# Kernel optimization log

Hardware: AMD Instinct MI355X
Metric: run time of the kernel (lower is better)

Reference implementation:

```python
import jax, jax.numpy as jnp
import numpy as np
jax.config.update("jax_enable_x64", True)

MS_H = 10
MS_W = 10
EPS = 1e-8


def _window_mean(x, kh, kw):
    # x: [B, H, W]; VALID avg-pool with kernel (kh, kw), stride 1, via integral image
    c = jnp.cumsum(jnp.cumsum(x, axis=1), axis=2)
    c = jnp.pad(c, ((0, 0), (1, 0), (1, 0)))
    H, W = x.shape[1], x.shape[2]
    oh, ow = H - kh + 1, W - kw + 1
    s = (c[:, kh:kh + oh, kw:kw + ow] - c[:, :oh, kw:kw + ow]
         - c[:, kh:kh + oh, :ow] + c[:, :oh, :ow])
    return s / (kh * kw)


def _translate_bilinear(imgs, dy, dx):
    # imgs: [B, H, W]; out[b,i,j] = imgs[b, i - dy[b], j - dx[b]] (bilinear, zero fill)
    B, H, W = imgs.shape
    yq = jnp.arange(H, dtype=imgs.dtype)[None, :, None] - dy[:, None, None]
    xq = jnp.arange(W, dtype=imgs.dtype)[None, None, :] - dx[:, None, None]
    y0 = jnp.floor(yq); x0 = jnp.floor(xq)
    wy = yq - y0;       wx = xq - x0
    y0i = y0.astype(jnp.int32); x0i = x0.astype(jnp.int32)
    b = jnp.arange(B)[:, None, None]
    def samp(yi, xi):
        valid = (yi >= 0) & (yi < H) & (xi >= 0) & (xi < W)
        v = imgs[b, jnp.clip(yi, 0, H - 1), jnp.clip(xi, 0, W - 1)]
        return jnp.where(valid, v, jnp.zeros((), imgs.dtype))
    v00 = samp(y0i, x0i);     v01 = samp(y0i, x0i + 1)
    v10 = samp(y0i + 1, x0i); v11 = samp(y0i + 1, x0i + 1)
    return (v00 * (1 - wy) * (1 - wx) + v01 * (1 - wy) * wx
            + v10 * wy * (1 - wx) + v11 * wy * wx)


def _motion_correct(fr, template):
    # fr: [1, B, H, W, 1] float32; template: [H, W] float32
    B = fr.shape[1]
    H, W = template.shape
    mx, my = H // 2, W // 2
    # --- template normalization ---
    t_zm = template - jnp.mean(template)
    t_var = jnp.sum(jnp.square(t_zm)) + EPS
    target_freq = jnp.fft.fft2(t_zm.astype(jnp.complex128))            # [H, W]
    imgs = fr[0, :, :, :, 0]                                           # [B, H, W]
    imgs_zm = imgs - jnp.mean(imgs, axis=(1, 2), keepdims=True)
    # --- local statistics (avg_pool2d VALID, kernel = template minus shift margins) ---
    kh, kw = H - 2 * MS_W, W - 2 * MS_H
    m1 = _window_mean(imgs, kh, kw)                                    # [B, 2mw+1, 2mh+1]
    m2 = _window_mean(jnp.square(imgs), kh, kw)
    imgs_var = m2 - jnp.square(m1) / (kh * kw) + EPS
    imgs_var = jnp.where(imgs_var < 0, 0.0, imgs_var)
    denominator = jnp.sqrt(t_var * imgs_var)
    # --- FFT cross-correlation (fft3d over batch+spatial, exactly as the TF code) ---
    fr_freq = jnp.fft.fftn(imgs_zm.astype(jnp.complex128), axes=(0, 1, 2))
    img_product = fr_freq * jnp.conj(target_freq)[None]
    cc = jnp.abs(jnp.fft.ifftn(img_product, axes=(0, 1, 2))).astype(jnp.float32)
    rolled = jnp.roll(cc, (B, mx, my), axis=(0, 1, 2))
    nom = rolled[:, mx - MS_W:mx + MS_W + 1, my - MS_H:my + MS_H + 1]
    ncc = nom / denominator
    ncc = jnp.where(jnp.isnan(ncc), 0.0, ncc)                          # [B, 2mw+1, 2mh+1]
    # --- integer peak ---
    flat = ncc.reshape(B, -1)
    am = jnp.argmax(flat, axis=1)
    shx = am // (2 * MS_H + 1)
    shy = am % (2 * MS_H + 1)
    sh_x_n = -(shx - MS_H).astype(jnp.float32)
    sh_y_n = -(shy - MS_W).astype(jnp.float32)
    # --- log-parabolic sub-pixel refinement ---
    l = jnp.log(ncc)
    b = jnp.arange(B)
    lxm1 = l[b, shx - 1, shy]; lxp1 = l[b, shx + 1, shy]
    lym1 = l[b, shx, shy - 1]; lyp1 = l[b, shx, shy + 1]
    lc4 = 4.0 * l[b, shx, shy]
    sh_x_n = sh_x_n - (lxm1 - lxp1) / (2 * lxm1 - lc4 + 2 * lxp1)
    sh_y_n = sh_y_n - (lym1 - lyp1) / (2 * lym1 - lc4 + 2 * lyp1)
    # --- bilinear translate; tfa translations = [sh_y (dx, width), sh_x (dy, height)] ---
    warped = _translate_bilinear(imgs, sh_x_n, sh_y_n)                 # [B, H, W]
    return jnp.transpose(warped, (0, 2, 1)).reshape(B, H * W)


def setup_inputs() -> dict:
    H = W = 512
    B = 32
    k1, k2, k3 = jax.random.split(jax.random.key(0), 3)
    # smooth (low-pass) random template so the NCC peak is smooth/positive around its max
    noise = jax.random.normal(k1, (H, W))
    f = jnp.sqrt(jnp.fft.fftfreq(H)[:, None] ** 2 + jnp.fft.fftfreq(W)[None, :] ** 2)
    lp = (f < 0.05).astype(jnp.complex128)
    template = jnp.real(jnp.fft.ifft2(jnp.fft.fft2(noise) * lp))
    template = (template / template.std()).astype(jnp.float32)
    # frames: template shifted by small random integer offsets + noise
    shifts = jax.random.randint(k2, (B, 2), -5, 6)
    frames = jax.vmap(lambda s: jnp.roll(template, (s[0], s[1]), axis=(0, 1)))(shifts)
    frames = frames + 0.05 * jax.random.normal(k3, (B, H, W), dtype=jnp.float32)
    fr = frames[None, :, :, :, None].astype(jnp.float32)
    return {"fr": fr, "template": template}


def reference(fr, template):
    return _motion_correct(fr, template)
```

## Files before the change

### kernel.cpp

```cpp
#include <hip/hip_runtime.h>
#include <math.h>

#define HH 512
#define WW 512
#define NPIX (HH*WW)
#define NB 32
#define NS 21
#define KWIN 492
#define NKB 512
#define MT28 28
#define PARTSZ (MT28*32*16)

typedef __attribute__((ext_vector_type(8))) short short8;
typedef __attribute__((ext_vector_type(8))) unsigned short ushort8;
typedef __attribute__((ext_vector_type(4))) float floatx4;

__device__ __forceinline__ unsigned short f2bf(float f) {
    unsigned u = __float_as_uint(f);
    unsigned r = (u + 0x7fffu + ((u >> 16) & 1u)) >> 16;
    return (unsigned short)r;
}

__global__ __launch_bounds__(256) void stage1(
    const float* __restrict__ fr, const float* __restrict__ tpl,
    unsigned short* __restrict__ tplv,
    float* __restrict__ I1, float* __restrict__ I2,
    double* __restrict__ sum1, double* __restrict__ sum2)
{
    int blk = blockIdx.x;
    int t   = threadIdx.x;
    if (blk < 512) {
        int id = blk;
        int b  = id >> 4;
        int yg = id & 15;
        int y0, ny;
        if (yg < 8) { y0 = 20 + 30 * yg; ny = 30; }
        else        { y0 = 260 + 29 * (yg - 8); ny = 29; }
        const float* img = fr + (size_t)b * NPIX;
        int xa = t, xb = t + 256;
        float s1a = 0.f, s2a = 0.f, s1b = 0.f, s2b = 0.f;
        for (int y = y0; y < y0 + ny; ++y) {
            float va = img[(size_t)y * WW + xa];
            float vb = img[(size_t)y * WW + xb];
            s1a += va; s2a += va * va;
            s1b += vb; s2b += vb * vb;
        }
        atomicAdd(&I1[b * WW + xa], s1a); atomicAdd(&I2[b * WW + xa], s2a);
        atomicAdd(&I1[b * WW + xb], s1b); atomicAdd(&I2[b * WW + xb], s2b);
    } else if (blk < 520) {
        int gq = blk - 512;
        int y0 = 64 * gq;
        int xa = t, xb = t + 256;
        float s1a = 0.f, s2a = 0.f, s1b = 0.f, s2b = 0.f;
        for (int y = y0; y < y0 + 64; ++y) {
            float va = tpl[(size_t)y * WW + xa];
            float vb = tpl[(size_t)y * WW + xb];
            s1a += va; s2a += va * va;
            s1b += vb; s2b += vb * vb;
        }
        double d1 = (double)s1a + (double)s1b;
        double d2 = (double)s2a + (double)s2b;
        for (int off = 32; off; off >>= 1) {
            d1 += __shfl_down(d1, off);
            d2 += __shfl_down(d2, off);
        }
        __shared__ double r1[4], r2[4];
        int lane = t & 63, wv = t >> 6;
        if (lane == 0) { r1[wv] = d1; r2[wv] = d2; }
        __syncthreads();
        if (t == 0) {
            atomicAdd(&sum1[32], r1[0] + r1[1] + r1[2] + r1[3]);
            atomicAdd(&sum2[32], r2[0] + r2[1] + r2[2] + r2[3]);
        }
    } else {
        int blk2 = blk - 520;
        int dv   = blk2 / 34;
        int prg  = blk2 % 34;
        int prEnd = min(16 * prg + 16, 532);
        int x2 = 2 * t;
        for (int pr = 16 * prg; pr < prEnd; ++pr) {
            int sy = (pr + 502) & 511;
            const float* srow = tpl + (size_t)sy * WW;
            unsigned short* drow = tplv + ((size_t)dv * 532 + pr) * 512;
            int sx0 = (x2     - dv + 522) & 511;
            int sx1 = (x2 + 1 - dv + 522) & 511;
            ushort2 o;
            o.x = f2bf(srow[sx0]);
            o.y = f2bf(srow[sx1]);
            *(ushort2*)(drow + x2) = o;
        }
    }
}

__global__ __launch_bounds__(896) void corr_mfma(
    const float* __restrict__ fr,
    const unsigned short* __restrict__ tplv,
    float* __restrict__ part)
{
    __shared__ unsigned short Bs[16384];

    const int t   = threadIdx.x;
    const int l   = t & 63;
    const int wid = t >> 6;
    const int idx = blockIdx.x;
    const int kb  = ((idx & 7) << 6) | (idx >> 3);
    const int k0  = kb << 9;
    const int kg  = l >> 4;
    const int ln  = l & 15;

    for (int i = t; i < 4096; i += 896) {
        int frame = i >> 7;
        int q     = i & 127;
        float4 v = *(const float4*)(fr + (size_t)frame * NPIX + k0 + 4 * q);
        int k8 = q >> 1, j4 = (q & 1) * 4;
        ushort4 o;
        o.x = f2bf(v.x); o.y = f2bf(v.y); o.z = f2bf(v.z); o.w = f2bf(v.w);
        *(ushort4*)&Bs[(k8 * 32 + frame) * 8 + j4] = o;
    }

    const unsigned short* pA0;
    const unsigned short* pA1;
    {
        int m_g = 32 * wid + ln;
        int du  = (m_g * 1561) >> 15;
        int dv  = m_g - 21 * du;
        if (m_g >= 441) { du = 0; dv = 0; }
        pA0 = tplv + ((size_t)(dv * 532 + 20 - du) * 512 + 8 * kg + k0);
        m_g = 32 * wid + 16 + ln;
        du  = (m_g * 1561) >> 15;
        dv  = m_g - 21 * du;
        if (m_g >= 441) { du = 0; dv = 0; }
        pA1 = tplv + ((size_t)(dv * 532 + 20 - du) * 512 + 8 * kg + k0);
    }

    const unsigned short* lB = Bs + kg * 256 + ln * 8;

    __syncthreads();

    floatx4 acc00 = {}, acc01 = {}, acc10 = {}, acc11 = {};

#pragma unroll
    for (int ks = 0; ks < 16; ++ks) {
        short8 A0 = *(const short8*)pA0;
        short8 A1 = *(const short8*)pA1;
        short8 B0 = *(const short8*)(lB + ks * 1024);
        short8 B1 = *(const short8*)(lB + ks * 1024 + 128);
        acc00 = __builtin_amdgcn_mfma_f32_16x16x32_bf16(A0, B0, acc00, 0, 0, 0);
        acc01 = __builtin_amdgcn_mfma_f32_16x16x32_bf16(A0, B1, acc01, 0, 0, 0);
        acc10 = __builtin_amdgcn_mfma_f32_16x16x32_bf16(A1, B0, acc10, 0, 0, 0);
        acc11 = __builtin_amdgcn_mfma_f32_16x16x32_bf16(A1, B1, acc11, 0, 0, 0);
        pA0 += 32; pA1 += 32;
    }

    {
        size_t base = ((size_t)kb * MT28 + 2 * wid) * 32;
        floatx4* p;
        p = (floatx4*)(part + (base + ln)      * 16 + 4 * kg); *p = acc00;
        p = (floatx4*)(part + (base + 16 + ln) * 16 + 4 * kg); *p = acc01;
        p = (floatx4*)(part + (base + 32 + ln) * 16 + 4 * kg); *p = acc10;
        p = (floatx4*)(part + (base + 48 + ln) * 16 + 4 * kg); *p = acc11;
    }
}

__global__ __launch_bounds__(512) void reduce_stage2(
    const float* __restrict__ part, float* __restrict__ cc,
    const float* __restrict__ fr, const float* __restrict__ I1,
    const float* __restrict__ I2, double* __restrict__ sum1,
    const double* __restrict__ sum2, float* __restrict__ denom)
{
    __shared__ double wr1[NS][8], wr2[NS][8], wrT[8];
    __shared__ float  e1[NS][40], e2[NS][40];
    __shared__ double totals1[NS], totals2[NS];

    int blk = blockIdx.x;
    if (blk < 224) {
        int oct = blk / 28;
        int j   = (blk % 28) * 512 + threadIdx.x;
        const float* p = part + (size_t)(oct * 64) * PARTSZ + j;
        float s = 0.f;
#pragma unroll 8
        for (int i = 0; i < 64; ++i)
            s += p[(size_t)i * PARTSZ];
        int mr    = j & 15;
        int n     = (j >> 4) & 31;
        int mtile = j >> 9;
        int m = mtile * 16 + mr;
        if (m < 441)
            atomicAdd(&cc[(size_t)n * 441 + m], s);
        return;
    }

    int b = blk - 224;
    int x = threadIdx.x;
    const float* img = fr + (size_t)b * NPIX;
    float top[20], bot[20];
#pragma unroll
    for (int y = 0; y < 20; ++y) top[y] = img[(size_t)y * WW + x];
#pragma unroll
    for (int y = 0; y < 20; ++y) bot[y] = img[(size_t)(492 + y) * WW + x];

    float t1 = 0.f, t2 = 0.f, b1 = 0.f, b2 = 0.f;
#pragma unroll
    for (int y = 0; y < 20; ++y) {
        t1 += top[y]; t2 += top[y] * top[y];
        b1 += bot[y]; b2 += bot[y] * bot[y];
    }
    float i1 = I1[b * WW + x], i2 = I2[b * WW + x];
    int lane = x & 63, wv = x >> 6;

    double tot = (double)i1 + (double)t1 + (double)b1;
    for (int off = 32; off; off >>= 1) tot += __shfl_down(tot, off);
    if (lane == 0) wrT[wv] = tot;

    float s1 = i1 + t1, s2 = i2 + t2;
#pragma unroll
    for (int u = 0; u < NS; ++u) {
        if (u) {
            float a = top[u-1], c = bot[u-1];
            s1 += c - a;
            s2 += c * c - a * a;
        }
        double d1 = (double)s1, d2 = (double)s2;
        for (int off = 32; off; off >>= 1) {
            d1 += __shfl_down(d1, off);
            d2 += __shfl_down(d2, off);
        }
        if (lane == 0) { wr1[u][wv] = d1; wr2[u][wv] = d2; }
        if (x < 20)        { e1[u][x]       = s1; e2[u][x]       = s2; }
        else if (x >= 492) { e1[u][x - 472] = s1; e2[u][x - 472] = s2; }
    }
    __syncthreads();
    if (x == 0) {
        double s = 0.0;
        for (int i = 0; i < 8; ++i) s += wrT[i];
        sum1[b] = s;
    }
    if (x < NS) {
        double a = 0.0, c = 0.0;
        for (int i = 0; i < 8; ++i) { a += wr1[x][i]; c += wr2[x][i]; }
        totals1[x] = a; totals2[x] = c;
    }
    __syncthreads();
    if (x < NS * NS) {
        int u = x / NS, v = x - NS * u;
        double S1 = totals1[u], S2 = totals2[u];
        for (int j = 0; j < v; ++j)  { S1 -= (double)e1[u][j];      S2 -= (double)e2[u][j]; }
        for (int j = v; j < 20; ++j) { S1 -= (double)e1[u][20 + j]; S2 -= (double)e2[u][20 + j]; }
        const double inv = 1.0 / ((double)KWIN * (double)KWIN);
        double m1 = S1 * inv, m2 = S2 * inv;
        double var = m2 - (m1 * m1) * inv + 1e-8;
        if (var < 0.0) var = 0.0;
        double tv = sum2[32] - sum1[32] * sum1[32] * (1.0 / (double)NPIX) + 1e-8;
        denom[(size_t)b * NS * NS + x] = (float)sqrt(tv * var);
    }
}

__global__ __launch_bounds__(64) void argmax_kernel(
    const float* __restrict__ cc, const float* __restrict__ denom,
    const double* __restrict__ sum1, float* __restrict__ shifts)
{
    int b = blockIdx.x;
    const float* C = cc    + (size_t)b * NS * NS;
    const float* D = denom + (size_t)b * NS * NS;
    float corr = (float)(sum1[b] * sum1[32] * (1.0 / (double)NPIX));
    int l = threadIdx.x;
    float best = -1e30f; int bidx = NS * NS;
    for (int i = l; i < NS * NS; i += 64) {
        float v = fabsf(C[i] - corr) / D[i];
        if (v != v) v = 0.f;
        if (v > best) { best = v; bidx = i; }
    }
    for (int off = 32; off; off >>= 1) {
        float ov = __shfl_down(best, off);
        int   oi = __shfl_down(bidx, off);
        if (ov > best || (ov == best && oi < bidx)) { best = ov; bidx = oi; }
    }
    if (l == 0) {
        int shx = bidx / NS, shy = bidx % NS;
        auto nccAt = [&](int i, int j) -> float {
            i = (i < 0) ? i + NS : i; i = (i > NS - 1) ? NS - 1 : i;
            j = (j < 0) ? j + NS : j; j = (j > NS - 1) ? NS - 1 : j;
            float v = fabsf(C[i * NS + j] - corr) / D[i * NS + j];
            if (v != v) v = 0.f;
            return v;
        };
        float lc  = logf(nccAt(shx, shy));
        float lxm = logf(nccAt(shx - 1, shy));
        float lxp = logf(nccAt(shx + 1, shy));
        float lym = logf(nccAt(shx, shy - 1));
        float lyp = logf(nccAt(shx, shy + 1));
        float shxn = -(float)(shx - 10) - (lxm - lxp) / (2.f * lxm - 4.f * lc + 2.f * lxp);
        float shyn = -(float)(shy - 10) - (lym - lyp) / (2.f * lym - 4.f * lc + 2.f * lyp);
        shifts[b]      = shxn;
        shifts[32 + b] = shyn;
    }
}

__device__ __forceinline__ float samp(const float* __restrict__ img, int y, int x) {
    bool valid = (y >= 0) & (y < HH) & (x >= 0) & (x < WW);
    int yc = min(max(y, 0), HH - 1), xc = min(max(x, 0), WW - 1);
    float v = img[(size_t)yc * WW + xc];
    return valid ? v : 0.f;
}

__global__ __launch_bounds__(256) void warp_kernel(
    const float* __restrict__ fr, const float* __restrict__ shifts,
    float* __restrict__ out)
{
    int b  = blockIdx.z;
    int h0 = blockIdx.y * 32;
    int w0 = blockIdx.x * 32;
    float dy = shifts[b], dx = shifts[32 + b];
    const float* img = fr + (size_t)b * NPIX;
    __shared__ float tile[32][33];
    int tx = threadIdx.x & 31;
    int tz = threadIdx.x >> 5;
#pragma unroll
    for (int s = 0; s < 4; ++s) {
        int h = h0 + tz + 8 * s;
        int w = w0 + tx;
        float yq = (float)h - dy;
        float xq = (float)w - dx;
        float y0f = floorf(yq), x0f = floorf(xq);
        float wy = yq - y0f, wx = xq - x0f;
        int y0 = (int)y0f, x0 = (int)x0f;
        float v00 = samp(img, y0,     x0);
        float v01 = samp(img, y0,     x0 + 1);
        float v10 = samp(img, y0 + 1, x0);
        float v11 = samp(img, y0 + 1, x0 + 1);
        float val = v00 * (1.f - wy) * (1.f - wx) + v01 * (1.f - wy) * wx
                  + v10 * wy * (1.f - wx)         + v11 * wy * wx;
        tile[tz + 8 * s][tx] = val;
    }
    __syncthreads();
#pragma unroll
    for (int s = 0; s < 4; ++s) {
        int hh = tx;
        int ww = tz + 8 * s;
        out[(size_t)b * NPIX + (size_t)(w0 + ww) * HH + (h0 + hh)] = tile[hh][ww];
    }
}

extern "C" void kernel_launch(void* const* d_in, const int* in_sizes, int n_in,
                              void* d_out, int out_size, void* d_ws, size_t ws_size,
                              hipStream_t stream) {
    const float* fr  = (const float*)d_in[0];
    const float* tpl = (const float*)d_in[1];
    float* out = (float*)d_out;
    char* ws = (char*)d_ws;

    double* sum1    = (double*)(ws + 0);
    double* sum2    = (double*)(ws + 512);
    float*  cc      = (float*) (ws + 4096);
    float*  I1      = (float*) (ws + 61440);
    float*  I2      = (float*) (ws + 126976);
    float*  shifts  = (float*) (ws + 196608);
    float*  denom   = (float*) (ws + 200704);
    unsigned short* tplv = (unsigned short*)(ws + 262144);
    float*  part    = (float*) (ws + 16777216);

    hipMemsetAsync(ws, 0, 192512, stream);

    stage1       <<<1234, 256, 0, stream>>>(fr, tpl, tplv, I1, I2, sum1, sum2);
    corr_mfma    <<<512, 896, 0, stream>>>(fr, tplv, part);
    reduce_stage2<<<256, 512, 0, stream>>>(part, cc, fr, I1, I2, sum1, sum2, denom);
    argmax_kernel<<<32, 64, 0, stream>>>(cc, denom, sum1, shifts);
    warp_kernel  <<<dim3(16, 16, 32), 256, 0, stream>>>(fr, shifts, out);
}
```

Baseline: 167.1 us.

## Shrink shifted-template buffer, drop memset and atomics, fuse argmax into reduce

The 21 column-shifted bf16 template copies are replaced by two parity copies with a 544-wide padded row. The MFMA A-operand loads now use 4-byte loads so that unaligned offsets are handled. Column and template sums become per-block partials summed later, which removes the memset and the float atomics. The argmax kernel is merged into the reduce kernel through a global flag spin-wait on the 224 reduce blocks, which saves one launch. The spin-wait depends on co-residency of the reduce blocks and the per-batch argmax blocks, and the cross-block handoff adds a risk of deadlock or stalls.

```diff
diff --git a/kernel.cpp b/kernel.cpp
--- a/kernel.cpp
+++ b/kernel.cpp
@@ -7,12 +7,11 @@
 #define NB 32
 #define NS 21
 #define KWIN 492
-#define NKB 512
 #define MT28 28
 #define PARTSZ (MT28*32*16)
+#define TPLB_COPY 278528
 
 typedef __attribute__((ext_vector_type(8))) short short8;
-typedef __attribute__((ext_vector_type(8))) unsigned short ushort8;
 typedef __attribute__((ext_vector_type(4))) float floatx4;
 
 __device__ __forceinline__ unsigned short f2bf(float f) {
@@ -21,80 +20,79 @@
     return (unsigned short)r;
 }
 
-__global__ __launch_bounds__(256) void stage1(
+__device__ __forceinline__ short8 loadA(const unsigned short* p) {
+    union { short8 v; unsigned u[4]; } r;
+    const unsigned* q = (const unsigned*)p;
+    r.u[0] = q[0]; r.u[1] = q[1]; r.u[2] = q[2]; r.u[3] = q[3];
+    return r.v;
+}
+
+__global__ __launch_bounds__(512) void prep(
     const float* __restrict__ fr, const float* __restrict__ tpl,
-    unsigned short* __restrict__ tplv,
-    float* __restrict__ I1, float* __restrict__ I2,
-    double* __restrict__ sum1, double* __restrict__ sum2)
+    unsigned short* __restrict__ tplb,
+    float* __restrict__ I1p, float* __restrict__ I2p,
+    double* __restrict__ tplS1p, double* __restrict__ tplS2p,
+    int* __restrict__ flag)
 {
     int blk = blockIdx.x;
     int t   = threadIdx.x;
-    if (blk < 512) {
-        int id = blk;
-        int b  = id >> 4;
-        int yg = id & 15;
-        int y0, ny;
-        if (yg < 8) { y0 = 20 + 30 * yg; ny = 30; }
-        else        { y0 = 260 + 29 * (yg - 8); ny = 29; }
+    if (blk == 0 && t == 0) *flag = 0;
+
+    if (blk < 256) {
+        int b = blk >> 3, oct = blk & 7;
         const float* img = fr + (size_t)b * NPIX;
-        int xa = t, xb = t + 256;
-        float s1a = 0.f, s2a = 0.f, s1b = 0.f, s2b = 0.f;
-        for (int y = y0; y < y0 + ny; ++y) {
-            float va = img[(size_t)y * WW + xa];
-            float vb = img[(size_t)y * WW + xb];
-            s1a += va; s2a += va * va;
-            s1b += vb; s2b += vb * vb;
-        }
-        atomicAdd(&I1[b * WW + xa], s1a); atomicAdd(&I2[b * WW + xa], s2a);
-        atomicAdd(&I1[b * WW + xb], s1b); atomicAdd(&I2[b * WW + xb], s2b);
-    } else if (blk < 520) {
-        int gq = blk - 512;
-        int y0 = 64 * gq;
-        int xa = t, xb = t + 256;
-        float s1a = 0.f, s2a = 0.f, s1b = 0.f, s2b = 0.f;
-        for (int y = y0; y < y0 + 64; ++y) {
-            float va = tpl[(size_t)y * WW + xa];
-            float vb = tpl[(size_t)y * WW + xb];
-            s1a += va; s2a += va * va;
-            s1b += vb; s2b += vb * vb;
-        }
-        double d1 = (double)s1a + (double)s1b;
-        double d2 = (double)s2a + (double)s2b;
+        int x = t;
+        float s1 = 0.f, s2 = 0.f;
+        int y0 = 20 + 59 * oct;
+        for (int y = y0; y < y0 + 59; ++y) {
+            float v = img[(size_t)y * WW + x];
+            s1 += v; s2 += v * v;
+        }
+        I1p[(size_t)blk * 512 + x] = s1;
+        I2p[(size_t)blk * 512 + x] = s2;
+    } else if (blk < 320) {
+        __shared__ double jb1[8], jb2[8];
+        int tj = blk - 256;
+        const float* trow = tpl + (size_t)tj * 8 * WW;
+        float s1 = 0.f, s2 = 0.f;
+        int x = t;
+        for (int y = 0; y < 8; ++y) {
+            float v = trow[(size_t)y * WW + x];
+            s1 += v; s2 += v * v;
+        }
+        double d1 = (double)s1, d2 = (double)s2;
         for (int off = 32; off; off >>= 1) {
             d1 += __shfl_down(d1, off);
             d2 += __shfl_down(d2, off);
         }
-        __shared__ double r1[4], r2[4];
         int lane = t & 63, wv = t >> 6;
-        if (lane == 0) { r1[wv] = d1; r2[wv] = d2; }
+        if (lane == 0) { jb1[wv] = d1; jb2[wv] = d2; }
         __syncthreads();
         if (t == 0) {
-            atomicAdd(&sum1[32], r1[0] + r1[1] + r1[2] + r1[3]);
-            atomicAdd(&sum2[32], r2[0] + r2[1] + r2[2] + r2[3]);
+            double a = 0.0, c = 0.0;
+            for (int i = 0; i < 8; ++i) { a += jb1[i]; c += jb2[i]; }
+            tplS1p[tj] = a; tplS2p[tj] = c;
         }
     } else {
-        int blk2 = blk - 520;
-        int dv   = blk2 / 34;
-        int prg  = blk2 % 34;
-        int prEnd = min(16 * prg + 16, 532);
-        int x2 = 2 * t;
-        for (int pr = 16 * prg; pr < prEnd; ++pr) {
-            int sy = (pr + 502) & 511;
+        int sy0 = (blk - 320) * 4;
+#pragma unroll
+        for (int rr = 0; rr < 4; ++rr) {
+            int sy = sy0 + rr;
             const float* srow = tpl + (size_t)sy * WW;
-            unsigned short* drow = tplv + ((size_t)dv * 532 + pr) * 512;
-            int sx0 = (x2     - dv + 522) & 511;
-            int sx1 = (x2 + 1 - dv + 522) & 511;
-            ushort2 o;
-            o.x = f2bf(srow[sx0]);
-            o.y = f2bf(srow[sx1]);
-            *(ushort2*)(drow + x2) = o;
+#pragma unroll
+            for (int P = 0; P < 2; ++P) {
+                for (int c = t; c < 544; c += 512) {
+                    int sx = (c + 496 - P) & 511;
+                    tplb[(size_t)P * TPLB_COPY + (size_t)sy * 544 + c] = f2bf(srow[sx]);
+                }
+            }
         }
     }
 }
 
 __global__ __launch_bounds__(896) void corr_mfma(
     const float* __restrict__ fr,
-    const unsigned short* __restrict__ tplv,
+    const unsigned short* __restrict__ tplb,
     float* __restrict__ part)
 {
     __shared__ unsigned short Bs[16384];
@@ -109,8 +107,7 @@
     const int ln  = l & 15;
 
     for (int i = t; i < 4096; i += 896) {
-        int frame = i >> 7;
-        int q     = i & 127;
+        int frame = i >> 7, q = i & 127;
         float4 v = *(const float4*)(fr + (size_t)frame * NPIX + k0 + 4 * q);
         int k8 = q >> 1, j4 = (q & 1) * 4;
         ushort4 o;
@@ -125,12 +122,16 @@
         int du  = (m_g * 1561) >> 15;
         int dv  = m_g - 21 * du;
         if (m_g >= 441) { du = 0; dv = 0; }
-        pA0 = tplv + ((size_t)(dv * 532 + 20 - du) * 512 + 8 * kg + k0);
+        int P   = dv & 1;
+        pA0 = tplb + (size_t)P * TPLB_COPY
+            + (size_t)((kb + 522 - du) & 511) * 544 + (8 * kg - dv + 26 + P);
         m_g = 32 * wid + 16 + ln;
         du  = (m_g * 1561) >> 15;
         dv  = m_g - 21 * du;
         if (m_g >= 441) { du = 0; dv = 0; }
-        pA1 = tplv + ((size_t)(dv * 532 + 20 - du) * 512 + 8 * kg + k0);
+        P   = dv & 1;
+        pA1 = tplb + (size_t)P * TPLB_COPY
+            + (size_t)((kb + 522 - du) & 511) * 544 + (8 * kg - dv + 26 + P);
     }
 
     const unsigned short* lB = Bs + kg * 256 + ln * 8;
@@ -141,8 +142,8 @@
 
 #pragma unroll
     for (int ks = 0; ks < 16; ++ks) {
-        short8 A0 = *(const short8*)pA0;
-        short8 A1 = *(const short8*)pA1;
+        short8 A0 = loadA(pA0);
+        short8 A1 = loadA(pA1);
         short8 B0 = *(const short8*)(lB + ks * 1024);
         short8 B1 = *(const short8*)(lB + ks * 1024 + 128);
         acc00 = __builtin_amdgcn_mfma_f32_16x16x32_bf16(A0, B0, acc00, 0, 0, 0);
@@ -162,36 +163,39 @@
     }
 }
 
-__global__ __launch_bounds__(512) void reduce_stage2(
-    const float* __restrict__ part, float* __restrict__ cc,
-    const float* __restrict__ fr, const float* __restrict__ I1,
-    const float* __restrict__ I2, double* __restrict__ sum1,
-    const double* __restrict__ sum2, float* __restrict__ denom)
+__global__ __launch_bounds__(512) void reduce_am(
+    const float* __restrict__ part, float* __restrict__ cc8,
+    const float* __restrict__ fr, const float* __restrict__ I1p,
+    const float* __restrict__ I2p, const double* __restrict__ tplS1p,
+    const double* __restrict__ tplS2p, int* __restrict__ flag,
+    float* __restrict__ shifts)
 {
-    __shared__ double wr1[NS][8], wr2[NS][8], wrT[8];
-    __shared__ float  e1[NS][40], e2[NS][40];
-    __shared__ double totals1[NS], totals2[NS];
-
     int blk = blockIdx.x;
+    int t   = threadIdx.x;
+
     if (blk < 224) {
         int oct = blk / 28;
-        int j   = (blk % 28) * 512 + threadIdx.x;
+        int j   = (blk % 28) * 512 + t;
         const float* p = part + (size_t)(oct * 64) * PARTSZ + j;
         float s = 0.f;
 #pragma unroll 8
         for (int i = 0; i < 64; ++i)
             s += p[(size_t)i * PARTSZ];
-        int mr    = j & 15;
-        int n     = (j >> 4) & 31;
-        int mtile = j >> 9;
-        int m = mtile * 16 + mr;
-        if (m < 441)
-            atomicAdd(&cc[(size_t)n * 441 + m], s);
+        cc8[(size_t)oct * PARTSZ + j] = s;
+        __threadfence();
+        __syncthreads();
+        if (t == 0) atomicAdd(flag, 1);
         return;
     }
 
+    __shared__ double wr1[NS][8], wr2[NS][8], wrT[8];
+    __shared__ float  e1[NS][40], e2[NS][40];
+    __shared__ double totals1[NS], totals2[NS];
+    __shared__ float  denomS[NS * NS];
+    __shared__ double tS1s, tS2s, sum1b;
+
     int b = blk - 224;
-    int x = threadIdx.x;
+    int x = t;
     const float* img = fr + (size_t)b * NPIX;
     float top[20], bot[20];
 #pragma unroll
@@ -205,8 +209,22 @@
         t1 += top[y]; t2 += top[y] * top[y];
         b1 += bot[y]; b2 += bot[y] * bot[y];
     }
-    float i1 = I1[b * WW + x], i2 = I2[b * WW + x];
+    float i1 = 0.f, i2 = 0.f;
+#pragma unroll
+    for (int o = 0; o < 8; ++o) {
+        i1 += I1p[((size_t)(b * 8 + o)) * 512 + x];
+        i2 += I2p[((size_t)(b * 8 + o)) * 512 + x];
+    }
     int lane = x & 63, wv = x >> 6;
+
+    if (x < 64) {
+        double d1 = tplS1p[x], d2 = tplS2p[x];
+        for (int off = 32; off; off >>= 1) {
+            d1 += __shfl_down(d1, off);
+            d2 += __shfl_down(d2, off);
+        }
+        if (x == 0) { tS1s = d1; tS2s = d2; }
+    }
 
     double tot = (double)i1 + (double)t1 + (double)b1;
     for (int off = 32; off; off >>= 1) tot += __shfl_down(tot, off);
@@ -233,7 +251,7 @@
     if (x == 0) {
         double s = 0.0;
         for (int i = 0; i < 8; ++i) s += wrT[i];
-        sum1[b] = s;
+        sum1b = s;
     }
     if (x < NS) {
         double a = 0.0, c = 0.0;
@@ -250,49 +268,58 @@
         double m1 = S1 * inv, m2 = S2 * inv;
         double var = m2 - (m1 * m1) * inv + 1e-8;
         if (var < 0.0) var = 0.0;
-        double tv = sum2[32] - sum1[32] * sum1[32] * (1.0 / (double)NPIX) + 1e-8;
-        denom[(size_t)b * NS * NS + x] = (float)sqrt(tv * var);
-    }
-}
-
-__global__ __launch_bounds__(64) void argmax_kernel(
-    const float* __restrict__ cc, const float* __restrict__ denom,
-    const double* __restrict__ sum1, float* __restrict__ shifts)
-{
-    int b = blockIdx.x;
-    const float* C = cc    + (size_t)b * NS * NS;
-    const float* D = denom + (size_t)b * NS * NS;
-    float corr = (float)(sum1[b] * sum1[32] * (1.0 / (double)NPIX));
-    int l = threadIdx.x;
-    float best = -1e30f; int bidx = NS * NS;
-    for (int i = l; i < NS * NS; i += 64) {
-        float v = fabsf(C[i] - corr) / D[i];
-        if (v != v) v = 0.f;
-        if (v > best) { best = v; bidx = i; }
-    }
-    for (int off = 32; off; off >>= 1) {
-        float ov = __shfl_down(best, off);
-        int   oi = __shfl_down(bidx, off);
-        if (ov > best || (ov == best && oi < bidx)) { best = ov; bidx = oi; }
-    }
-    if (l == 0) {
-        int shx = bidx / NS, shy = bidx % NS;
-        auto nccAt = [&](int i, int j) -> float {
-            i = (i < 0) ? i + NS : i; i = (i > NS - 1) ? NS - 1 : i;
-            j = (j < 0) ? j + NS : j; j = (j > NS - 1) ? NS - 1 : j;
-            float v = fabsf(C[i * NS + j] - corr) / D[i * NS + j];
+        double tv = tS2s - tS1s * tS1s * (1.0 / (double)NPIX) + 1e-8;
+        denomS[x] = (float)sqrt(tv * var);
+    }
+    __syncthreads();
+
+    if (t == 0) {
+        while (__hip_atomic_load(flag, __ATOMIC_ACQUIRE,
+                                 __HIP_MEMORY_SCOPE_AGENT) < 224)
+            __builtin_amdgcn_s_sleep(2);
+    }
+    __syncthreads();
+    __threadfence();
+
+    if (t < 64) {
+        float corr = (float)(sum1b * tS1s * (1.0 / (double)NPIX));
+        auto ccAt = [&](int m) -> float {
+            int jj = ((m >> 4) * 512) + b * 16 + (m & 15);
+            float s = 0.f;
+#pragma unroll
+            for (int o = 0; o < 8; ++o) s += cc8[(size_t)o * PARTSZ + jj];
+            return s;
+        };
+        float best = -1e30f; int bidx = NS * NS;
+        for (int i = t; i < NS * NS; i += 64) {
+            float v = fabsf(ccAt(i) - corr) / denomS[i];
             if (v != v) v = 0.f;
-            return v;
-        };
-        float lc  = logf(nccAt(shx, shy));
-        float lxm = logf(nccAt(shx - 1, shy));
-        float lxp = logf(nccAt(shx + 1, shy));
-        float lym = logf(nccAt(shx, shy - 1));
-        float lyp = logf(nccAt(shx, shy + 1));
-        float shxn = -(float)(shx - 10) - (lxm - lxp) / (2.f * lxm - 4.f * lc + 2.f * lxp);
-        float shyn = -(float)(shy - 10) - (lym - lyp) / (2.f * lym - 4.f * lc + 2.f * lyp);
-        shifts[b]      = shxn;
-        shifts[32 + b] = shyn;
+            if (v > best) { best = v; bidx = i; }
+        }
+        for (int off = 32; off; off >>= 1) {
+            float ov = __shfl_down(best, off);
+            int   oi = __shfl_down(bidx, off);
+            if (ov > best || (ov == best && oi < bidx)) { best = ov; bidx = oi; }
+        }
+        if (t == 0) {
+            int shx = bidx / NS, shy = bidx % NS;
+            auto nccAt = [&](int i, int j) -> float {
+                i = (i < 0) ? i + NS : i; i = (i > NS - 1) ? NS - 1 : i;
+                j = (j < 0) ? j + NS : j; j = (j > NS - 1) ? NS - 1 : j;
+                float v = fabsf(ccAt(i * NS + j) - corr) / denomS[i * NS + j];
+                if (v != v) v = 0.f;
+                return v;
+            };
+            float lc  = logf(nccAt(shx, shy));
+            float lxm = logf(nccAt(shx - 1, shy));
+            float lxp = logf(nccAt(shx + 1, shy));
+            float lym = logf(nccAt(shx, shy - 1));
+            float lyp = logf(nccAt(shx, shy + 1));
+            float shxn = -(float)(shx - 10) - (lxm - lxp) / (2.f * lxm - 4.f * lc + 2.f * lxp);
+            float shyn = -(float)(shy - 10) - (lym - lyp) / (2.f * lym - 4.f * lc + 2.f * lyp);
+            shifts[b]      = shxn;
+            shifts[32 + b] = shyn;
+        }
     }
 }
 
@@ -349,21 +376,18 @@
     float* out = (float*)d_out;
     char* ws = (char*)d_ws;
 
-    double* sum1    = (double*)(ws + 0);
-    double* sum2    = (double*)(ws + 512);
-    float*  cc      = (float*) (ws + 4096);
-    float*  I1      = (float*) (ws + 61440);
-    float*  I2      = (float*) (ws + 126976);
-    float*  shifts  = (float*) (ws + 196608);
-    float*  denom   = (float*) (ws + 200704);
-    unsigned short* tplv = (unsigned short*)(ws + 262144);
-    float*  part    = (float*) (ws + 16777216);
-
-    hipMemsetAsync(ws, 0, 192512, stream);
-
-    stage1       <<<1234, 256, 0, stream>>>(fr, tpl, tplv, I1, I2, sum1, sum2);
-    corr_mfma    <<<512, 896, 0, stream>>>(fr, tplv, part);
-    reduce_stage2<<<256, 512, 0, stream>>>(part, cc, fr, I1, I2, sum1, sum2, denom);
-    argmax_kernel<<<32, 64, 0, stream>>>(cc, denom, sum1, shifts);
-    warp_kernel  <<<dim3(16, 16, 32), 256, 0, stream>>>(fr, shifts, out);
-}
+    unsigned short* tplb = (unsigned short*)(ws + 0);
+    float*  I1p    = (float*) (ws + 2097152);
+    float*  I2p    = (float*) (ws + 2621440);
+    double* tplS1p = (double*)(ws + 3145728);
+    double* tplS2p = (double*)(ws + 3146240);
+    float*  shifts = (float*) (ws + 3146752);
+    int*    flag   = (int*)   (ws + 3147264);
+    float*  cc8    = (float*) (ws + 4194304);
+    float*  part   = (float*) (ws + 8388608);
+
+    prep     <<<448, 512, 0, stream>>>(fr, tpl, tplb, I1p, I2p, tplS1p, tplS2p, flag);
+    corr_mfma<<<512, 896, 0, stream>>>(fr, tplb, part);
+    reduce_am<<<256, 512, 0, stream>>>(part, cc8, fr, I1p, I2p, tplS1p, tplS2p, flag, shifts);
+    warp_kernel<<<dim3(16, 16, 32), 256, 0, stream>>>(fr, shifts, out);
+}
```

After: 177.6 us. 1.06x slower.
